# Optimization experiments

Hardware: AMD Instinct MI355X
Metric: run time of the kernel (lower is better)

The kernel has to match this reference:

```python
import jax, jax.numpy as jnp
import numpy as np

FEATURES_DIM = 100000
NUM_FIELDS = 39
EMBED_DIM = 64
DIM_INT = (2, 3)
RANK = (32, 32)
BATCH = 8192


def setup_inputs() -> dict:
    key = jax.random.key(0)
    ks = jax.random.split(key, 6)
    x = jax.random.randint(ks[0], (BATCH, NUM_FIELDS), 0, FEATURES_DIM)
    embed_table = jax.random.normal(ks[1], (FEATURES_DIM, EMBED_DIM), dtype=jnp.float32) * 0.01
    linear_w = jax.random.normal(ks[2], (FEATURES_DIM, 1), dtype=jnp.float32) * 0.01
    linear_bias = jnp.zeros((1,), dtype=jnp.float32)
    # trunc_normal_(std=0.01) approximated by clipped normal
    W0 = jnp.clip(jax.random.normal(ks[3], (DIM_INT[0], RANK[0], NUM_FIELDS), dtype=jnp.float32) * 0.01, -0.02, 0.02)
    W1 = jnp.clip(jax.random.normal(ks[4], (DIM_INT[1], RANK[1], NUM_FIELDS), dtype=jnp.float32) * 0.01, -0.02, 0.02)
    return {"x": x, "embed_table": embed_table, "linear_w": linear_w,
            "linear_bias": linear_bias, "W0": W0, "W1": W1}


def _calc_cross(W, emb):
    # W: (l, j, k) = (dim_int, rank, num_fields); emb: (b, k, i) = (batch, fields, embed)
    # dot_products[b,i,j,l] = sum_k W[l,j,k] * emb[b,k,i]
    dp = jnp.einsum('ljk,bki->bijl', W, emb)          # (b, embed, rank, dim_int)
    prod_over_l = jnp.prod(dp, axis=3)                # (b, embed, rank)
    return jnp.sum(prod_over_l, axis=(1, 2))          # (b,)


def reference(x, embed_table, linear_w, linear_bias, W0, W1):
    emb = embed_table[x]                              # (b, fields, embed)
    lin = jnp.sum(linear_w[x], axis=1) + linear_bias  # (b, 1)
    ret = lin[:, 0] + _calc_cross(W0, emb) + _calc_cross(W1, emb)
    return ret                                        # (b,)
```

## Files before the change

### kernel.cpp

```cpp
#include <hip/hip_runtime.h>
#include <hip/hip_bf16.h>

#define BATCH    8192
#define NF       39
#define ED       64
#define RANK     32
#define NL       5
#define KP       48
#define KH       56
#define SPW      4

typedef _Float16 half8  __attribute__((ext_vector_type(8)));
typedef float    f32x16 __attribute__((ext_vector_type(16)));

__global__ __launch_bounds__(256, 2) void tfm_kernel(
    const int*   __restrict__ x,
    const float* __restrict__ embed,
    const float* __restrict__ linw,
    const float* __restrict__ lbias,
    const float* __restrict__ W0,
    const float* __restrict__ W1,
    float*       __restrict__ out)
{
    __shared__ __align__(16) _Float16 Es[4][ED][KH];

    const int t    = threadIdx.x;
    const int lane = t & 63;
    const int w    = t >> 6;
    const int gw   = blockIdx.x * 4 + w;
    const int s0   = gw * SPW;

    const float bias = lbias[0];

    int xv[SPW];
#pragma unroll
    for (int si = 0; si < SPW; ++si)
        xv[si] = (lane < NF) ? x[(s0 + si) * NF + lane] : 0;

    const int j  = lane & 31;
    const int kh = lane >> 5;
    half8 wf[NL][3];
#pragma unroll
    for (int l = 0; l < NL; ++l) {
        const float* base = (l < 2) ? (W0 + (l * RANK + j) * NF)
                                    : (W1 + ((l - 2) * RANK + j) * NF);
#pragma unroll
        for (int kc = 0; kc < 3; ++kc) {
#pragma unroll
            for (int e = 0; e < 8; ++e) {
                int k = kc * 16 + kh * 8 + e;
                wf[l][kc][e] = (k < NF) ? (_Float16)base[k] : (_Float16)0.0f;
            }
        }
    }

#pragma unroll
    for (int si = 0; si < SPW; ++si) {
        const int s = s0 + si;

        float lv = 0.0f;
        if (lane < NF) lv = linw[xv[si]];

        float r[NF];
#pragma unroll
        for (int k = 0; k < NF; ++k) {
            int xi = __builtin_amdgcn_readlane(xv[si], k);
            const float* rowp = embed + (size_t)xi * ED;
            r[k] = rowp[lane];
        }

#pragma unroll
        for (int c6 = 0; c6 < 6; ++c6) {
            half8 hh;
#pragma unroll
            for (int e = 0; e < 8; ++e) {
                int k = c6 * 8 + e;
                hh[e] = (k < NF) ? (_Float16)r[k] : (_Float16)0.0f;
            }
            *(half8*)&Es[w][lane][c6 * 8] = hh;
        }

        float ssum = lv;

#pragma unroll
        for (int tile = 0; tile < 2; ++tile) {
            f32x16 acc[NL];
#pragma unroll
            for (int l = 0; l < NL; ++l)
#pragma unroll
                for (int e = 0; e < 16; ++e) acc[l][e] = 0.0f;

            const int c = tile * 32 + (lane & 31);
#pragma unroll
            for (int kc = 0; kc < 3; ++kc) {
                half8 bf = *(const half8*)&Es[w][c][kc * 16 + kh * 8];
#pragma unroll
                for (int l = 0; l < NL; ++l)
                    acc[l] = __builtin_amdgcn_mfma_f32_32x32x16_f16(
                                 wf[l][kc], bf, acc[l], 0, 0, 0);
            }
#pragma unroll
            for (int e = 0; e < 16; ++e) {
                ssum += acc[0][e] * acc[1][e];
                ssum += acc[2][e] * acc[3][e] * acc[4][e];
            }
        }

#pragma unroll
        for (int off = 32; off > 0; off >>= 1) ssum += __shfl_down(ssum, off, 64);
        if (lane == 0) out[s] = ssum + bias;
    }
}

extern "C" void kernel_launch(void* const* d_in, const int* in_sizes, int n_in,
                              void* d_out, int out_size, void* d_ws, size_t ws_size,
                              hipStream_t stream) {
    const int*   x     = (const int*)  d_in[0];
    const float* embed = (const float*)d_in[1];
    const float* linw  = (const float*)d_in[2];
    const float* lbias = (const float*)d_in[3];
    const float* W0    = (const float*)d_in[4];
    const float* W1    = (const float*)d_in[5];
    float*       out   = (float*)d_out;

    tfm_kernel<<<BATCH / (4 * SPW), 256, 0, stream>>>(x, embed, linw, lbias, W0, W1, out);
}
```

Measured before the change: 95.42 us.

## Halve samples per wave and split MFMA accumulators to raise occupancy

Reduces samples per wave from four to two, doubling the grid, and raises the launch-bounds occupancy target to three blocks per CU. The five concurrent MFMA accumulators are split into a pair group and a triple group so fewer accumulator registers are live at once. The linear-weight gathers are hoisted ahead of the loop and the LDS row stride is padded to 72 halves. More waves should hide gather latency better, at the cost of a possible partial tail wave and fewer samples to amortize the W fragment loads.

Result: slower. 102.7 us (+7.6%).

```diff
diff --git a/kernel.cpp b/kernel.cpp
--- a/kernel.cpp
+++ b/kernel.cpp
@@ -5,15 +5,13 @@
 #define NF       39
 #define ED       64
 #define RANK     32
-#define NL       5
-#define KP       48
-#define KH       56
-#define SPW      4
+#define SPW      2
+#define KST      72
 
 typedef _Float16 half8  __attribute__((ext_vector_type(8)));
 typedef float    f32x16 __attribute__((ext_vector_type(16)));
 
-__global__ __launch_bounds__(256, 2) void tfm_kernel(
+__global__ __launch_bounds__(256, 3) void tfm_kernel(
     const int*   __restrict__ x,
     const float* __restrict__ embed,
     const float* __restrict__ linw,
@@ -22,51 +20,48 @@
     const float* __restrict__ W1,
     float*       __restrict__ out)
 {
-    __shared__ __align__(16) _Float16 Es[4][ED][KH];
+    __shared__ __align__(16) _Float16 Es[4][ED][KST];
 
     const int t    = threadIdx.x;
     const int lane = t & 63;
     const int w    = t >> 6;
-    const int gw   = blockIdx.x * 4 + w;
-    const int s0   = gw * SPW;
+    const int s0   = (blockIdx.x * 4 + w) * SPW;
 
     const float bias = lbias[0];
+    const int j  = lane & 31;
+    const int kh = lane >> 5;
 
     int xv[SPW];
 #pragma unroll
     for (int si = 0; si < SPW; ++si)
         xv[si] = (lane < NF) ? x[(s0 + si) * NF + lane] : 0;
 
-    const int j  = lane & 31;
-    const int kh = lane >> 5;
-    half8 wf[NL][3];
+    float lv[SPW];
 #pragma unroll
-    for (int l = 0; l < NL; ++l) {
+    for (int si = 0; si < SPW; ++si)
+        lv[si] = (lane < NF) ? linw[xv[si]] : 0.0f;
+
+    half8 wf[5][3];
+#pragma unroll
+    for (int l = 0; l < 5; ++l) {
         const float* base = (l < 2) ? (W0 + (l * RANK + j) * NF)
                                     : (W1 + ((l - 2) * RANK + j) * NF);
 #pragma unroll
-        for (int kc = 0; kc < 3; ++kc) {
+        for (int kc = 0; kc < 3; ++kc)
 #pragma unroll
             for (int e = 0; e < 8; ++e) {
                 int k = kc * 16 + kh * 8 + e;
                 wf[l][kc][e] = (k < NF) ? (_Float16)base[k] : (_Float16)0.0f;
             }
-        }
     }
 
 #pragma unroll
     for (int si = 0; si < SPW; ++si) {
-        const int s = s0 + si;
-
-        float lv = 0.0f;
-        if (lane < NF) lv = linw[xv[si]];
-
         float r[NF];
 #pragma unroll
         for (int k = 0; k < NF; ++k) {
             int xi = __builtin_amdgcn_readlane(xv[si], k);
-            const float* rowp = embed + (size_t)xi * ED;
-            r[k] = rowp[lane];
+            r[k] = embed[(size_t)xi * ED + lane];
         }
 
 #pragma unroll
@@ -80,35 +75,46 @@
             *(half8*)&Es[w][lane][c6 * 8] = hh;
         }
 
-        float ssum = lv;
+        float ssum = lv[si];
 
 #pragma unroll
         for (int tile = 0; tile < 2; ++tile) {
-            f32x16 acc[NL];
+            const int c = tile * 32 + j;
+            half8 bf[3];
 #pragma unroll
-            for (int l = 0; l < NL; ++l)
+            for (int kc = 0; kc < 3; ++kc)
+                bf[kc] = *(const half8*)&Es[w][c][kc * 16 + kh * 8];
+
+            {
+                f32x16 a0, a1;
 #pragma unroll
-                for (int e = 0; e < 16; ++e) acc[l][e] = 0.0f;
-
-            const int c = tile * 32 + (lane & 31);
+                for (int e = 0; e < 16; ++e) { a0[e] = 0.0f; a1[e] = 0.0f; }
 #pragma unroll
-            for (int kc = 0; kc < 3; ++kc) {
-                half8 bf = *(const half8*)&Es[w][c][kc * 16 + kh * 8];
+                for (int kc = 0; kc < 3; ++kc) {
+                    a0 = __builtin_amdgcn_mfma_f32_32x32x16_f16(wf[0][kc], bf[kc], a0, 0, 0, 0);
+                    a1 = __builtin_amdgcn_mfma_f32_32x32x16_f16(wf[1][kc], bf[kc], a1, 0, 0, 0);
+                }
 #pragma unroll
-                for (int l = 0; l < NL; ++l)
-                    acc[l] = __builtin_amdgcn_mfma_f32_32x32x16_f16(
-                                 wf[l][kc], bf, acc[l], 0, 0, 0);
+                for (int e = 0; e < 16; ++e) ssum += a0[e] * a1[e];
             }
+            {
+                f32x16 c0, c1, c2;
 #pragma unroll
-            for (int e = 0; e < 16; ++e) {
-                ssum += acc[0][e] * acc[1][e];
-                ssum += acc[2][e] * acc[3][e] * acc[4][e];
+                for (int e = 0; e < 16; ++e) { c0[e] = 0.0f; c1[e] = 0.0f; c2[e] = 0.0f; }
+#pragma unroll
+                for (int kc = 0; kc < 3; ++kc) {
+                    c0 = __builtin_amdgcn_mfma_f32_32x32x16_f16(wf[2][kc], bf[kc], c0, 0, 0, 0);
+                    c1 = __builtin_amdgcn_mfma_f32_32x32x16_f16(wf[3][kc], bf[kc], c1, 0, 0, 0);
+                    c2 = __builtin_amdgcn_mfma_f32_32x32x16_f16(wf[4][kc], bf[kc], c2, 0, 0, 0);
+                }
+#pragma unroll
+                for (int e = 0; e < 16; ++e) ssum += c0[e] * c1[e] * c2[e];
             }
         }
 
 #pragma unroll
         for (int off = 32; off > 0; off >>= 1) ssum += __shfl_down(ssum, off, 64);
-        if (lane == 0) out[s] = ssum + bias;
+        if (lane == 0) out[s0 + si] = ssum + bias;
     }
 }
 
```
